# Optimization experiments

Measured on AMD Instinct MI355X. Metric: run time of the kernel, lower is better.

The kernel has to match this reference:

```python
import jax, jax.numpy as jnp
import numpy as np

LAMBDA_SOFTMAX = 10.0  # opt.lambda_softmax
LEAKY_SLOPE = 0.1


def l2norm(x, axis):
    # matches torch F.normalize(p=2, eps=1e-12)
    n = jnp.linalg.norm(x, axis=axis, keepdims=True)
    return x / jnp.clip(n, 1e-12)


def setup_inputs() -> dict:
    key = jax.random.key(0)
    k1, k2, k3, k4, k5 = jax.random.split(key, 5)
    I, Q, T, S, D = 64, 49, 64, 64, 256  # n_img, n_region, n_txt, max_words, feature_size
    return {
        "local_img_query": jax.random.normal(k1, (I, Q, D), jnp.float32),
        "local_img_value": jax.random.normal(k2, (I, Q, D), jnp.float32),
        "local_text_key": jax.random.normal(k3, (T, S, D), jnp.float32),
        "local_text_value": jax.random.normal(k4, (T, S, D), jnp.float32),
        "text_length": jax.random.randint(k5, (T,), 8, S + 1, jnp.int32),
    }


def reference(local_img_query, local_img_value, local_text_key, local_text_value, text_length):
    # Vectorized form of the per-sentence Python loop in compute_i2t_sim.
    # Variable sentence lengths are handled with a mask over the padded word axis,
    # which reproduces the ragged torch math exactly (see comments).
    T, S, D = local_text_key.shape
    I, Q, _ = local_img_query.shape

    qn = l2norm(local_img_query, -1)   # [I,Q,D]
    kn = l2norm(local_text_key, -1)    # [T,S,D]

    # bmm(txt_key_norm, queryT): (B,S,D)x(B,D,Q) -> here [T,I,S,Q]
    attn = jnp.einsum('tsd,iqd->tisq', kn, qn)
    attn = jnp.where(attn > 0, attn, LEAKY_SLOPE * attn)      # LeakyReLU(0.1)
    # l2norm(attn, 2) normalizes over queryL per (t,i,s) row -> independent of padding
    attn = l2norm(attn, -1)
    attn = jnp.swapaxes(attn, 2, 3)                            # [T,I,Q,S]

    mask = jnp.arange(S)[None, :] < text_length[:, None]       # [T,S]
    logits = jnp.where(mask[:, None, None, :], attn * LAMBDA_SOFTMAX, -jnp.inf)
    attn = jax.nn.softmax(logits, axis=-1)                     # padded words -> exactly 0

    # focal_equal with sourceL = actual n_word of each sentence
    n_word = text_length.astype(attn.dtype)[:, None, None, None]
    funcF = attn * n_word - jnp.sum(attn, axis=-1, keepdims=True)
    fattn = (funcF > 0).astype(attn.dtype)                     # padded attn=0 -> funcF<0 -> 0
    tmp = fattn * attn
    attn = tmp / jnp.sum(tmp, axis=-1, keepdims=True)

    # bmm(valueT, attnT) -> weighted text context per (txt, img): [T,I,Q,D]
    wei = jnp.einsum('tsd,tiqs->tiqd', local_text_value, attn)
    wei = l2norm(wei, -1)

    # cosine similarity with image values along d, then mean over regions
    v = local_img_value[None]                                  # [1,I,Q,D]
    w12 = jnp.sum(v * wei, -1)
    denom = jnp.linalg.norm(v, axis=-1) * jnp.linalg.norm(wei, axis=-1)
    sim = w12 / jnp.clip(denom, 1e-8)                          # [T,I,Q]
    i2t = sim.mean(axis=-1)                                    # [T,I]
    return i2t.T                                               # [n_img, n_txt]
```

## Files before the change

kernel.cpp:

```cpp
#include <hip/hip_runtime.h>
#include <math.h>

#define I_N 64
#define Q_N 49
#define T_N 64
#define S_N 64
#define D_N 256

typedef __attribute__((ext_vector_type(8))) short short8;
typedef __attribute__((ext_vector_type(4))) float f32x4;
typedef unsigned short ushort_t;

__device__ __forceinline__ float waveReduceSum64(float v) {
    v += __shfl_xor(v, 1);
    v += __shfl_xor(v, 2);
    v += __shfl_xor(v, 4);
    v += __shfl_xor(v, 8);
    v += __shfl_xor(v, 16);
    v += __shfl_xor(v, 32);
    return v;
}

__device__ __forceinline__ ushort_t f2bf(float x) {
    unsigned u = __builtin_bit_cast(unsigned, x);
    unsigned r = (u + 0x7fffu + ((u >> 16) & 1u)) >> 16;
    return (ushort_t)r;
}
__device__ __forceinline__ float bf2f(ushort_t h) {
    unsigned u = ((unsigned)h) << 16;
    return __builtin_bit_cast(float, u);
}
__device__ __forceinline__ void split_bf16(float x, ushort_t& h, ushort_t& l) {
    h = f2bf(x);
    l = f2bf(x - bf2f(h));
}

__global__ void prep_all(const float* __restrict__ q_in, const float* __restrict__ v_in,
                         const float* __restrict__ k_in, const float* __restrict__ tv,
                         ushort_t* __restrict__ qfh, ushort_t* __restrict__ qfl,
                         ushort_t* __restrict__ kfh, ushort_t* __restrict__ kfl,
                         ushort_t* __restrict__ vfh, ushort_t* __restrict__ vfl,
                         float* __restrict__ vP, float* __restrict__ vnorm) {
    __shared__ float tile[64][65];
    __shared__ float ws[8];
    int b = blockIdx.x;
    int tid = threadIdx.x;

    if (b < 8192) {
        int isimg = (b < 4096) ? 1 : 0;
        int row = isimg ? b : (b - 4096);
        int hi = row >> 6, lo = row & 63;
        float x = 0.0f, vv = 0.0f;
        if (isimg) {
            if (lo < Q_N) {
                size_t base = ((size_t)hi * Q_N + lo) * D_N + tid;
                x = q_in[base];
                vv = v_in[base];
            }
        } else {
            x = k_in[(size_t)row * D_N + tid];
        }
        float s1 = waveReduceSum64(x * x);
        float s2 = waveReduceSum64(vv * vv);
        int wv = tid >> 6, ln = tid & 63;
        if (ln == 0) { ws[wv] = s1; ws[4 + wv] = s2; }
        __syncthreads();
        float n1 = sqrtf(ws[0] + ws[1] + ws[2] + ws[3]);
        float xn = x / fmaxf(n1, 1e-12f);
        ushort_t h, l;
        split_bf16(xn, h, l);
        size_t off = ((size_t)hi << 14) + (size_t)((((lo >> 4) * 8 + (tid >> 5))) << 9)
                   + (size_t)(((((tid >> 3) & 3) * 16 + (lo & 15))) << 3) + (tid & 7);
        if (isimg) {
            qfh[off] = h;
            qfl[off] = l;
            if (tid == 0) vnorm[row] = sqrtf(ws[4] + ws[5] + ws[6] + ws[7]);
        } else {
            kfh[off] = h;
            kfl[off] = l;
        }
    } else if (b < 8448) {
        int bb = b - 8192;
        int t = bb >> 2;
        int d0 = (bb & 3) * 64;
        const float* src = tv + ((size_t)t << 14) + d0;
        ushort_t* dh = vfh + ((size_t)t << 14);
        ushort_t* dl = vfl + ((size_t)t << 14);
#pragma unroll
        for (int r = 0; r < 16; ++r) {
            int idx = r * 256 + tid;
            int s = idx >> 6, d = idx & 63;
            tile[s][d] = src[s * D_N + d];
        }
        __syncthreads();
#pragma unroll
        for (int r = 0; r < 16; ++r) {
            int idx = r * 256 + tid;
            int d = idx >> 6, s = idx & 63;
            int dg = d0 + d;
            float x = tile[s][d];
            ushort_t h, l;
            split_bf16(x, h, l);
            int dgrp = dg >> 4, lrd = dg & 15;
            int k0g = s >> 5, lk3 = (s >> 3) & 3, e = s & 7;
            size_t off = (size_t)(dgrp << 10) + (k0g << 9) + ((lk3 * 16 + lrd) << 3) + e;
            dh[off] = h;
            dl[off] = l;
        }
    } else {
        int i = b - 8448;
        const float* src = v_in + (size_t)i * Q_N * D_N;
        int wv = tid >> 6, lane = tid & 63;
        int lr = lane & 15, lk = lane >> 4;
        float* d0 = vP + ((size_t)i << 14) + (size_t)tid * 64;
#pragma unroll
        for (int nq = 0; nq < 4; ++nq) {
            int q = nq * 16 + lr;
#pragma unroll
            for (int md = 0; md < 4; ++md)
#pragma unroll
                for (int r = 0; r < 4; ++r) {
                    int d = wv * 64 + md * 16 + lk * 4 + r;
                    d0[nq * 16 + md * 4 + r] = (q < Q_N) ? src[q * D_N + d] : 0.0f;
                }
        }
    }
}

__launch_bounds__(256, 3)
__global__ void i2t_mfma(const ushort_t* __restrict__ kfh, const ushort_t* __restrict__ kfl,
                         const ushort_t* __restrict__ qfh, const ushort_t* __restrict__ qfl,
                         const ushort_t* __restrict__ vfh, const ushort_t* __restrict__ vfl,
                         const float* __restrict__ vP,
                         const float* __restrict__ vnorm,
                         const int* __restrict__ tlen,
                         float* __restrict__ out)
{
    __shared__ __align__(16) unsigned char RK[33280];

    const int bid = blockIdx.x;
    const int xcd = bid & 7;
    const int j = bid >> 3;
    const int t = (xcd << 3) | (j & 7);
    const int i = j >> 3;

    const int tid = threadIdx.x;
    const int lane = tid & 63;
    const int w = tid >> 6;
    const int lr = lane & 15;
    const int lk = lane >> 4;

    const int wsr = (w >> 1) * 32;
    const int wq  = (w & 1) * 32;
    f32x4 acc[2][2];
#pragma unroll
    for (int a = 0; a < 2; ++a)
#pragma unroll
        for (int b2 = 0; b2 < 2; ++b2) acc[a][b2] = (f32x4){0.f, 0.f, 0.f, 0.f};
    {
        const ushort_t* kH = kfh + ((size_t)t << 14) + (size_t)(w >> 1) * 8192;
        const ushort_t* kL = kfl + ((size_t)t << 14) + (size_t)(w >> 1) * 8192;
        const ushort_t* qH = qfh + ((size_t)i << 14) + (size_t)(w & 1) * 8192;
        const ushort_t* qL = qfl + ((size_t)i << 14) + (size_t)(w & 1) * 8192;
#pragma unroll
        for (int k8 = 0; k8 < 8; ++k8) {
            int fo = k8 * 512 + lane * 8;
            short8 aH0 = *(const short8*)(kH + fo);
            short8 aL0 = *(const short8*)(kL + fo);
            short8 aH1 = *(const short8*)(kH + 4096 + fo);
            short8 aL1 = *(const short8*)(kL + 4096 + fo);
            short8 bH0 = *(const short8*)(qH + fo);
            short8 bL0 = *(const short8*)(qL + fo);
            short8 bH1 = *(const short8*)(qH + 4096 + fo);
            short8 bL1 = *(const short8*)(qL + 4096 + fo);
            acc[0][0] = __builtin_amdgcn_mfma_f32_16x16x32_bf16(aH0, bH0, acc[0][0], 0, 0, 0);
            acc[0][1] = __builtin_amdgcn_mfma_f32_16x16x32_bf16(aH0, bH1, acc[0][1], 0, 0, 0);
            acc[1][0] = __builtin_amdgcn_mfma_f32_16x16x32_bf16(aH1, bH0, acc[1][0], 0, 0, 0);
            acc[1][1] = __builtin_amdgcn_mfma_f32_16x16x32_bf16(aH1, bH1, acc[1][1], 0, 0, 0);
            acc[0][0] = __builtin_amdgcn_mfma_f32_16x16x32_bf16(aH0, bL0, acc[0][0], 0, 0, 0);
            acc[0][1] = __builtin_amdgcn_mfma_f32_16x16x32_bf16(aH0, bL1, acc[0][1], 0, 0, 0);
            acc[1][0] = __builtin_amdgcn_mfma_f32_16x16x32_bf16(aH1, bL0, acc[1][0], 0, 0, 0);
            acc[1][1] = __builtin_amdgcn_mfma_f32_16x16x32_bf16(aH1, bL1, acc[1][1], 0, 0, 0);
            acc[0][0] = __builtin_amdgcn_mfma_f32_16x16x32_bf16(aL0, bH0, acc[0][0], 0, 0, 0);
            acc[0][1] = __builtin_amdgcn_mfma_f32_16x16x32_bf16(aL0, bH1, acc[0][1], 0, 0, 0);
            acc[1][0] = __builtin_amdgcn_mfma_f32_16x16x32_bf16(aL1, bH0, acc[1][0], 0, 0, 0);
            acc[1][1] = __builtin_amdgcn_mfma_f32_16x16x32_bf16(aL1, bH1, acc[1][1], 0, 0, 0);
        }
    }
    {
        float* As = (float*)RK;
#pragma unroll
        for (int si = 0; si < 2; ++si)
#pragma unroll
            for (int qi = 0; qi < 2; ++qi)
#pragma unroll
                for (int r = 0; r < 4; ++r) {
                    int s = wsr + si * 16 + lk * 4 + r;
                    int q = wq + qi * 16 + lr;
                    float v = acc[si][qi][r];
                    v = (v > 0.0f) ? v : 0.1f * v;
                    As[s * 65 + q] = v;
                }
    }
    __syncthreads();

    {
        const float* As = (const float*)RK;
        float* rinv = (float*)(RK + 16640);
        int s = tid >> 2, part = tid & 3;
        float ss = 0.0f;
#pragma unroll
        for (int q0 = 0; q0 < 64; q0 += 4) {
            float v = As[s * 65 + q0 + part];
            ss += v * v;
        }
        ss += __shfl_xor(ss, 1);
        ss += __shfl_xor(ss, 2);
        if (part == 0) rinv[s] = 1.0f / fmaxf(sqrtf(ss), 1e-12f);
    }
    __syncthreads();

    const int len = tlen[t];
    {
        const float* As = (const float*)RK;
        const float* rinv = (const float*)(RK + 16640);
        ushort_t* Ph = (ushort_t*)(RK + 16896);
        ushort_t* Pl = (ushort_t*)(RK + 25088);
        const float thr = 1.0f / (float)len;
        int q = tid >> 2, part = tid & 3;
        float logit[16];
        float m = -INFINITY;
#pragma unroll
        for (int k = 0; k < 16; ++k) {
            int s = part * 16 + k;
            float lg = (s < len) ? 10.0f * As[s * 65 + q] * rinv[s] : -INFINITY;
            logit[k] = lg;
            m = fmaxf(m, lg);
        }
        m = fmaxf(m, __shfl_xor(m, 1));
        m = fmaxf(m, __shfl_xor(m, 2));
        float p[16];
        float sum = 0.0f;
#pragma unroll
        for (int k = 0; k < 16; ++k) {
            int s = part * 16 + k;
            float e = (s < len) ? __expf(logit[k] - m) : 0.0f;
            p[k] = e;
            sum += e;
        }
        sum += __shfl_xor(sum, 1);
        sum += __shfl_xor(sum, 2);
        float inv = 1.0f / sum;
        float sk = 0.0f;
#pragma unroll
        for (int k = 0; k < 16; ++k) {
            p[k] *= inv;
            if (p[k] > thr) sk += p[k];
        }
        sk += __shfl_xor(sk, 1);
        sk += __shfl_xor(sk, 2);
        float iv2 = 1.0f / sk;

        ushort_t hh[16], ll[16];
#pragma unroll
        for (int k = 0; k < 16; ++k) {
            float pv = (p[k] > thr) ? p[k] * iv2 : 0.0f;
            if (q >= Q_N) pv = 0.0f;
            split_bf16(pv, hh[k], ll[k]);
        }
        int c0 = (2 * part) ^ (q & 7);
        int c1 = (2 * part + 1) ^ (q & 7);
        short8 v0, v1;
#pragma unroll
        for (int k = 0; k < 8; ++k) { v0[k] = (short)hh[k]; v1[k] = (short)hh[k + 8]; }
        *(short8*)(Ph + q * 64 + (c0 << 3)) = v0;
        *(short8*)(Ph + q * 64 + (c1 << 3)) = v1;
#pragma unroll
        for (int k = 0; k < 8; ++k) { v0[k] = (short)ll[k]; v1[k] = (short)ll[k + 8]; }
        *(short8*)(Pl + q * 64 + (c0 << 3)) = v0;
        *(short8*)(Pl + q * 64 + (c1 << 3)) = v1;
    }
    __syncthreads();

    f32x4 acc2[4][4];
#pragma unroll
    for (int a = 0; a < 4; ++a)
#pragma unroll
        for (int b2 = 0; b2 < 4; ++b2) acc2[a][b2] = (f32x4){0.f, 0.f, 0.f, 0.f};
    {
        const ushort_t* vH = vfh + ((size_t)t << 14) + (size_t)w * 4096;
        const ushort_t* vL = vfl + ((size_t)t << 14) + (size_t)w * 4096;
        const ushort_t* PH = (const ushort_t*)(RK + 16896);
        const ushort_t* PL = (const ushort_t*)(RK + 25088);
#pragma unroll
        for (int k0g = 0; k0g < 2; ++k0g) {
#pragma unroll
            for (int md = 0; md < 4; ++md) {
                int vo = md * 1024 + k0g * 512 + lane * 8;
                short8 vh = *(const short8*)(vH + vo);
                short8 vl = *(const short8*)(vL + vo);
#pragma unroll
                for (int nq = 0; nq < 4; ++nq) {
                    int qrow = nq * 16 + lr;
                    int o = qrow * 64 + (((k0g * 4 + lk) ^ (qrow & 7)) << 3);
                    short8 ph = *(const short8*)(PH + o);
                    short8 pl = *(const short8*)(PL + o);
                    acc2[md][nq] = __builtin_amdgcn_mfma_f32_16x16x32_bf16(vh, ph, acc2[md][nq], 0, 0, 0);
                    acc2[md][nq] = __builtin_amdgcn_mfma_f32_16x16x32_bf16(vl, ph, acc2[md][nq], 0, 0, 0);
                    acc2[md][nq] = __builtin_amdgcn_mfma_f32_16x16x32_bf16(vh, pl, acc2[md][nq], 0, 0, 0);
                }
            }
        }
    }

    {
        float* wsq = (float*)RK;
        float* wdv = (float*)(RK + 1024);
        const float* vPb = vP + ((((size_t)i * 4 + w) * 64 + lane) << 6);
#pragma unroll
        for (int nq = 0; nq < 4; ++nq) {
            float s2 = 0.0f, dv = 0.0f;
#pragma unroll
            for (int md = 0; md < 4; ++md) {
                f32x4 vv = *(const f32x4*)(vPb + nq * 16 + md * 4);
#pragma unroll
                for (int r = 0; r < 4; ++r) {
                    float wv = acc2[md][nq][r];
                    s2 += wv * wv;
                    dv += wv * vv[r];
                }
            }
            s2 += __shfl_xor(s2, 16);
            s2 += __shfl_xor(s2, 32);
            dv += __shfl_xor(dv, 16);
            dv += __shfl_xor(dv, 32);
            if (lane < 16) {
                wsq[w * 64 + nq * 16 + lane] = s2;
                wdv[w * 64 + nq * 16 + lane] = dv;
            }
        }
    }
    __syncthreads();
    if (tid < 64) {
        const float* wsq = (const float*)RK;
        const float* wdv = (const float*)(RK + 1024);
        int q = tid;
        float s2 = 0.0f, dv = 0.0f;
#pragma unroll
        for (int ww = 0; ww < 4; ++ww) {
            s2 += wsq[ww * 64 + q];
            dv += wdv[ww * 64 + q];
        }
        float sim = 0.0f;
        if (q < Q_N) {
            float wn = sqrtf(s2);
            float w12 = dv / fmaxf(wn, 1e-12f);
            float wnn = wn / fmaxf(wn, 1e-12f);
            float denom = fmaxf(vnorm[i * 64 + q] * wnn, 1e-8f);
            sim = w12 / denom;
        }
        sim = waveReduceSum64(sim);
        if (tid == 0) out[(size_t)i * T_N + t] = sim * (1.0f / (float)Q_N);
    }
}

extern "C" void kernel_launch(void* const* d_in, const int* in_sizes, int n_in,
                              void* d_out, int out_size, void* d_ws, size_t ws_size,
                              hipStream_t stream) {
    const float* img_query = (const float*)d_in[0];
    const float* img_value = (const float*)d_in[1];
    const float* text_key  = (const float*)d_in[2];
    const float* text_val  = (const float*)d_in[3];
    const int*   text_len  = (const int*)d_in[4];
    float* out = (float*)d_out;

    const size_t NPAD = (size_t)64 * 64 * 256;
    ushort_t* qfh = (ushort_t*)d_ws;
    ushort_t* qfl = qfh + NPAD;
    ushort_t* kfh = qfl + NPAD;
    ushort_t* kfl = kfh + NPAD;
    ushort_t* vfh = kfl + NPAD;
    ushort_t* vfl = vfh + NPAD;
    float* vnorm  = (float*)(vfl + NPAD);
    float* vP     = vnorm + I_N * 64;

    prep_all<<<8512, 256, 0, stream>>>(img_query, img_value, text_key, text_val,
                                       qfh, qfl, kfh, kfl, vfh, vfl, vP, vnorm);

    i2t_mfma<<<T_N * I_N, 256, 0, stream>>>(kfh, kfl, qfh, qfl, vfh, vfl,
                                            vP, vnorm, text_len, out);
}
```

Before: 116.1 us.

## Collapse per-pair block to a single wave with register-resident softmax

The 256-thread block per (text, image) pair becomes a single 64-lane wave. That wave computes the full 64x64 attention tile in MFMA accumulators. LeakyReLU, the row l2norm, the masked softmax and the focal threshold are all done in registers with cross-lane shuffles, so the fp32 staging of attention in LDS and all __syncthreads go away. The second GEMM is looped over four d-chunks inside the wave, and the cosine partials are accumulated in registers. The cost is more serial MFMA work and higher register pressure per wave, with fewer waves available to hide latency.

Result: slower. 126.8 us (+9.2%).

```diff
diff --git a/kernel.cpp b/kernel.cpp
--- a/kernel.cpp
+++ b/kernel.cpp
@@ -8,6 +8,7 @@
 #define D_N 256
 
 typedef __attribute__((ext_vector_type(8))) short short8;
+typedef __attribute__((ext_vector_type(4))) short s16x4;
 typedef __attribute__((ext_vector_type(4))) float f32x4;
 typedef unsigned short ushort_t;
 
@@ -127,8 +128,10 @@
     }
 }
 
-__launch_bounds__(256, 3)
-__global__ void i2t_mfma(const ushort_t* __restrict__ kfh, const ushort_t* __restrict__ kfl,
+#define MFMA16(A, B, C) __builtin_amdgcn_mfma_f32_16x16x32_bf16(A, B, C, 0, 0, 0)
+
+__launch_bounds__(64, 3)
+__global__ void i2t_wave(const ushort_t* __restrict__ kfh, const ushort_t* __restrict__ kfl,
                          const ushort_t* __restrict__ qfh, const ushort_t* __restrict__ qfl,
                          const ushort_t* __restrict__ vfh, const ushort_t* __restrict__ vfl,
                          const float* __restrict__ vP,
@@ -136,7 +139,8 @@
                          const int* __restrict__ tlen,
                          float* __restrict__ out)
 {
-    __shared__ __align__(16) unsigned char RK[33280];
+    __shared__ __align__(16) ushort_t Ph[4096];
+    __shared__ __align__(16) ushort_t Pl[4096];
 
     const int bid = blockIdx.x;
     const int xcd = bid & 7;
@@ -144,213 +148,208 @@
     const int t = (xcd << 3) | (j & 7);
     const int i = j >> 3;
 
-    const int tid = threadIdx.x;
-    const int lane = tid & 63;
-    const int w = tid >> 6;
-    const int lr = lane & 15;
-    const int lk = lane >> 4;
-
-    const int wsr = (w >> 1) * 32;
-    const int wq  = (w & 1) * 32;
-    f32x4 acc[2][2];
-#pragma unroll
-    for (int a = 0; a < 2; ++a)
-#pragma unroll
-        for (int b2 = 0; b2 < 2; ++b2) acc[a][b2] = (f32x4){0.f, 0.f, 0.f, 0.f};
+    const int l = threadIdx.x;
+    const int c16 = l & 15;
+    const int g = l >> 4;
+
+    f32x4 acc[4][4];
+#pragma unroll
+    for (int a = 0; a < 4; ++a)
+#pragma unroll
+        for (int b2 = 0; b2 < 4; ++b2) acc[a][b2] = (f32x4){0.f, 0.f, 0.f, 0.f};
     {
-        const ushort_t* kH = kfh + ((size_t)t << 14) + (size_t)(w >> 1) * 8192;
-        const ushort_t* kL = kfl + ((size_t)t << 14) + (size_t)(w >> 1) * 8192;
-        const ushort_t* qH = qfh + ((size_t)i << 14) + (size_t)(w & 1) * 8192;
-        const ushort_t* qL = qfl + ((size_t)i << 14) + (size_t)(w & 1) * 8192;
+        const ushort_t* kH = kfh + ((size_t)t << 14) + l * 8;
+        const ushort_t* kL = kfl + ((size_t)t << 14) + l * 8;
+        const ushort_t* qH = qfh + ((size_t)i << 14) + l * 8;
+        const ushort_t* qL = qfl + ((size_t)i << 14) + l * 8;
 #pragma unroll
         for (int k8 = 0; k8 < 8; ++k8) {
-            int fo = k8 * 512 + lane * 8;
-            short8 aH0 = *(const short8*)(kH + fo);
-            short8 aL0 = *(const short8*)(kL + fo);
-            short8 aH1 = *(const short8*)(kH + 4096 + fo);
-            short8 aL1 = *(const short8*)(kL + 4096 + fo);
-            short8 bH0 = *(const short8*)(qH + fo);
-            short8 bL0 = *(const short8*)(qL + fo);
-            short8 bH1 = *(const short8*)(qH + 4096 + fo);
-            short8 bL1 = *(const short8*)(qL + 4096 + fo);
-            acc[0][0] = __builtin_amdgcn_mfma_f32_16x16x32_bf16(aH0, bH0, acc[0][0], 0, 0, 0);
-            acc[0][1] = __builtin_amdgcn_mfma_f32_16x16x32_bf16(aH0, bH1, acc[0][1], 0, 0, 0);
-            acc[1][0] = __builtin_amdgcn_mfma_f32_16x16x32_bf16(aH1, bH0, acc[1][0], 0, 0, 0);
-            acc[1][1] = __builtin_amdgcn_mfma_f32_16x16x32_bf16(aH1, bH1, acc[1][1], 0, 0, 0);
-            acc[0][0] = __builtin_amdgcn_mfma_f32_16x16x32_bf16(aH0, bL0, acc[0][0], 0, 0, 0);
-            acc[0][1] = __builtin_amdgcn_mfma_f32_16x16x32_bf16(aH0, bL1, acc[0][1], 0, 0, 0);
-            acc[1][0] = __builtin_amdgcn_mfma_f32_16x16x32_bf16(aH1, bL0, acc[1][0], 0, 0, 0);
-            acc[1][1] = __builtin_amdgcn_mfma_f32_16x16x32_bf16(aH1, bL1, acc[1][1], 0, 0, 0);
-            acc[0][0] = __builtin_amdgcn_mfma_f32_16x16x32_bf16(aL0, bH0, acc[0][0], 0, 0, 0);
-            acc[0][1] = __builtin_amdgcn_mfma_f32_16x16x32_bf16(aL0, bH1, acc[0][1], 0, 0, 0);
-            acc[1][0] = __builtin_amdgcn_mfma_f32_16x16x32_bf16(aL1, bH0, acc[1][0], 0, 0, 0);
-            acc[1][1] = __builtin_amdgcn_mfma_f32_16x16x32_bf16(aL1, bH1, acc[1][1], 0, 0, 0);
-        }
-    }
+            short8 bH[4], bL[4];
+#pragma unroll
+            for (int qi = 0; qi < 4; ++qi) {
+                int o = (qi * 8 + k8) * 512;
+                bH[qi] = *(const short8*)(qH + o);
+                bL[qi] = *(const short8*)(qL + o);
+            }
+#pragma unroll
+            for (int si = 0; si < 4; ++si) {
+                int o = (si * 8 + k8) * 512;
+                short8 aH = *(const short8*)(kH + o);
+                short8 aL = *(const short8*)(kL + o);
+#pragma unroll
+                for (int qi = 0; qi < 4; ++qi) {
+                    acc[si][qi] = MFMA16(aH, bH[qi], acc[si][qi]);
+                    acc[si][qi] = MFMA16(aH, bL[qi], acc[si][qi]);
+                    acc[si][qi] = MFMA16(aL, bH[qi], acc[si][qi]);
+                }
+            }
+        }
+    }
+
+    const int len = tlen[t];
+    const float thr = 1.0f / (float)len;
+#pragma unroll
+    for (int si = 0; si < 4; ++si)
+#pragma unroll
+        for (int qi = 0; qi < 4; ++qi)
+#pragma unroll
+            for (int r = 0; r < 4; ++r) {
+                float v = acc[si][qi][r];
+                acc[si][qi][r] = (v > 0.0f) ? v : 0.1f * v;
+            }
     {
-        float* As = (float*)RK;
-#pragma unroll
-        for (int si = 0; si < 2; ++si)
-#pragma unroll
-            for (int qi = 0; qi < 2; ++qi)
-#pragma unroll
-                for (int r = 0; r < 4; ++r) {
-                    int s = wsr + si * 16 + lk * 4 + r;
-                    int q = wq + qi * 16 + lr;
+        float rv[4][4];
+#pragma unroll
+        for (int si = 0; si < 4; ++si)
+#pragma unroll
+            for (int r = 0; r < 4; ++r) {
+                float ss = 0.0f;
+#pragma unroll
+                for (int qi = 0; qi < 4; ++qi) {
                     float v = acc[si][qi][r];
-                    v = (v > 0.0f) ? v : 0.1f * v;
-                    As[s * 65 + q] = v;
-                }
-    }
-    __syncthreads();
-
-    {
-        const float* As = (const float*)RK;
-        float* rinv = (float*)(RK + 16640);
-        int s = tid >> 2, part = tid & 3;
-        float ss = 0.0f;
-#pragma unroll
-        for (int q0 = 0; q0 < 64; q0 += 4) {
-            float v = As[s * 65 + q0 + part];
-            ss += v * v;
-        }
-        ss += __shfl_xor(ss, 1);
-        ss += __shfl_xor(ss, 2);
-        if (part == 0) rinv[s] = 1.0f / fmaxf(sqrtf(ss), 1e-12f);
-    }
-    __syncthreads();
-
-    const int len = tlen[t];
-    {
-        const float* As = (const float*)RK;
-        const float* rinv = (const float*)(RK + 16640);
-        ushort_t* Ph = (ushort_t*)(RK + 16896);
-        ushort_t* Pl = (ushort_t*)(RK + 25088);
-        const float thr = 1.0f / (float)len;
-        int q = tid >> 2, part = tid & 3;
-        float logit[16];
+                    ss += v * v;
+                }
+                ss += __shfl_xor(ss, 1);
+                ss += __shfl_xor(ss, 2);
+                ss += __shfl_xor(ss, 4);
+                ss += __shfl_xor(ss, 8);
+                rv[si][r] = 10.0f / fmaxf(sqrtf(ss), 1e-12f);
+            }
+#pragma unroll
+        for (int si = 0; si < 4; ++si)
+#pragma unroll
+            for (int qi = 0; qi < 4; ++qi)
+#pragma unroll
+                for (int r = 0; r < 4; ++r) acc[si][qi][r] *= rv[si][r];
+    }
+#pragma unroll
+    for (int qi = 0; qi < 4; ++qi) {
         float m = -INFINITY;
 #pragma unroll
-        for (int k = 0; k < 16; ++k) {
-            int s = part * 16 + k;
-            float lg = (s < len) ? 10.0f * As[s * 65 + q] * rinv[s] : -INFINITY;
-            logit[k] = lg;
-            m = fmaxf(m, lg);
-        }
-        m = fmaxf(m, __shfl_xor(m, 1));
-        m = fmaxf(m, __shfl_xor(m, 2));
-        float p[16];
+        for (int si = 0; si < 4; ++si)
+#pragma unroll
+            for (int r = 0; r < 4; ++r) {
+                int s = si * 16 + g * 4 + r;
+                float lg = (s < len) ? acc[si][qi][r] : -INFINITY;
+                m = fmaxf(m, lg);
+            }
+        m = fmaxf(m, __shfl_xor(m, 16));
+        m = fmaxf(m, __shfl_xor(m, 32));
         float sum = 0.0f;
 #pragma unroll
-        for (int k = 0; k < 16; ++k) {
-            int s = part * 16 + k;
-            float e = (s < len) ? __expf(logit[k] - m) : 0.0f;
-            p[k] = e;
-            sum += e;
-        }
-        sum += __shfl_xor(sum, 1);
-        sum += __shfl_xor(sum, 2);
+        for (int si = 0; si < 4; ++si)
+#pragma unroll
+            for (int r = 0; r < 4; ++r) {
+                int s = si * 16 + g * 4 + r;
+                float e = (s < len) ? __expf(acc[si][qi][r] - m) : 0.0f;
+                acc[si][qi][r] = e;
+                sum += e;
+            }
+        sum += __shfl_xor(sum, 16);
+        sum += __shfl_xor(sum, 32);
         float inv = 1.0f / sum;
         float sk = 0.0f;
 #pragma unroll
-        for (int k = 0; k < 16; ++k) {
-            p[k] *= inv;
-            if (p[k] > thr) sk += p[k];
-        }
-        sk += __shfl_xor(sk, 1);
-        sk += __shfl_xor(sk, 2);
+        for (int si = 0; si < 4; ++si)
+#pragma unroll
+            for (int r = 0; r < 4; ++r) {
+                float p = acc[si][qi][r] * inv;
+                acc[si][qi][r] = p;
+                if (p > thr) sk += p;
+            }
+        sk += __shfl_xor(sk, 16);
+        sk += __shfl_xor(sk, 32);
         float iv2 = 1.0f / sk;
-
-        ushort_t hh[16], ll[16];
-#pragma unroll
-        for (int k = 0; k < 16; ++k) {
-            float pv = (p[k] > thr) ? p[k] * iv2 : 0.0f;
-            if (q >= Q_N) pv = 0.0f;
-            split_bf16(pv, hh[k], ll[k]);
-        }
-        int c0 = (2 * part) ^ (q & 7);
-        int c1 = (2 * part + 1) ^ (q & 7);
-        short8 v0, v1;
-#pragma unroll
-        for (int k = 0; k < 8; ++k) { v0[k] = (short)hh[k]; v1[k] = (short)hh[k + 8]; }
-        *(short8*)(Ph + q * 64 + (c0 << 3)) = v0;
-        *(short8*)(Ph + q * 64 + (c1 << 3)) = v1;
-#pragma unroll
-        for (int k = 0; k < 8; ++k) { v0[k] = (short)ll[k]; v1[k] = (short)ll[k + 8]; }
-        *(short8*)(Pl + q * 64 + (c0 << 3)) = v0;
-        *(short8*)(Pl + q * 64 + (c1 << 3)) = v1;
-    }
-    __syncthreads();
-
-    f32x4 acc2[4][4];
-#pragma unroll
-    for (int a = 0; a < 4; ++a)
-#pragma unroll
-        for (int b2 = 0; b2 < 4; ++b2) acc2[a][b2] = (f32x4){0.f, 0.f, 0.f, 0.f};
+        bool qok = (qi * 16 + c16) < Q_N;
+#pragma unroll
+        for (int si = 0; si < 4; ++si)
+#pragma unroll
+            for (int r = 0; r < 4; ++r) {
+                float p = acc[si][qi][r];
+                p = (p > thr) ? p * iv2 : 0.0f;
+                if (!qok) p = 0.0f;
+                acc[si][qi][r] = p;
+            }
+    }
+
+#pragma unroll
+    for (int si = 0; si < 4; ++si)
+#pragma unroll
+        for (int qi = 0; qi < 4; ++qi) {
+            int q = qi * 16 + c16;
+            int s0 = si * 16 + g * 4;
+            int cidx = s0 >> 3;
+            int off = q * 64 + ((cidx ^ (q & 7)) << 3) + (g & 1) * 4;
+            s16x4 vh, vl;
+#pragma unroll
+            for (int r = 0; r < 4; ++r) {
+                ushort_t hh, ll;
+                split_bf16(acc[si][qi][r], hh, ll);
+                vh[r] = (short)hh;
+                vl[r] = (short)ll;
+            }
+            *(s16x4*)(Ph + off) = vh;
+            *(s16x4*)(Pl + off) = vl;
+        }
+    __asm__ volatile("s_waitcnt lgkmcnt(0)" ::: "memory");
+    __builtin_amdgcn_sched_barrier(0);
+
+    float s2a[4] = {0.f, 0.f, 0.f, 0.f}, dva[4] = {0.f, 0.f, 0.f, 0.f};
     {
-        const ushort_t* vH = vfh + ((size_t)t << 14) + (size_t)w * 4096;
-        const ushort_t* vL = vfl + ((size_t)t << 14) + (size_t)w * 4096;
-        const ushort_t* PH = (const ushort_t*)(RK + 16896);
-        const ushort_t* PL = (const ushort_t*)(RK + 25088);
-#pragma unroll
-        for (int k0g = 0; k0g < 2; ++k0g) {
-#pragma unroll
-            for (int md = 0; md < 4; ++md) {
-                int vo = md * 1024 + k0g * 512 + lane * 8;
-                short8 vh = *(const short8*)(vH + vo);
-                short8 vl = *(const short8*)(vL + vo);
-#pragma unroll
-                for (int nq = 0; nq < 4; ++nq) {
-                    int qrow = nq * 16 + lr;
-                    int o = qrow * 64 + (((k0g * 4 + lk) ^ (qrow & 7)) << 3);
-                    short8 ph = *(const short8*)(PH + o);
-                    short8 pl = *(const short8*)(PL + o);
-                    acc2[md][nq] = __builtin_amdgcn_mfma_f32_16x16x32_bf16(vh, ph, acc2[md][nq], 0, 0, 0);
-                    acc2[md][nq] = __builtin_amdgcn_mfma_f32_16x16x32_bf16(vl, ph, acc2[md][nq], 0, 0, 0);
-                    acc2[md][nq] = __builtin_amdgcn_mfma_f32_16x16x32_bf16(vh, pl, acc2[md][nq], 0, 0, 0);
-                }
-            }
-        }
-    }
-
-    {
-        float* wsq = (float*)RK;
-        float* wdv = (float*)(RK + 1024);
-        const float* vPb = vP + ((((size_t)i * 4 + w) * 64 + lane) << 6);
-#pragma unroll
-        for (int nq = 0; nq < 4; ++nq) {
-            float s2 = 0.0f, dv = 0.0f;
-#pragma unroll
-            for (int md = 0; md < 4; ++md) {
-                f32x4 vv = *(const f32x4*)(vPb + nq * 16 + md * 4);
-#pragma unroll
-                for (int r = 0; r < 4; ++r) {
-                    float wv = acc2[md][nq][r];
-                    s2 += wv * wv;
-                    dv += wv * vv[r];
-                }
-            }
-            s2 += __shfl_xor(s2, 16);
-            s2 += __shfl_xor(s2, 32);
-            dv += __shfl_xor(dv, 16);
-            dv += __shfl_xor(dv, 32);
-            if (lane < 16) {
-                wsq[w * 64 + nq * 16 + lane] = s2;
-                wdv[w * 64 + nq * 16 + lane] = dv;
-            }
-        }
-    }
-    __syncthreads();
-    if (tid < 64) {
-        const float* wsq = (const float*)RK;
-        const float* wdv = (const float*)(RK + 1024);
-        int q = tid;
-        float s2 = 0.0f, dv = 0.0f;
-#pragma unroll
-        for (int ww = 0; ww < 4; ++ww) {
-            s2 += wsq[ww * 64 + q];
-            dv += wdv[ww * 64 + q];
-        }
+        const ushort_t* vH = vfh + ((size_t)t << 14) + l * 8;
+        const ushort_t* vL = vfl + ((size_t)t << 14) + l * 8;
+#pragma unroll
+        for (int dc = 0; dc < 4; ++dc) {
+            f32x4 acc2[4][4];
+#pragma unroll
+            for (int a = 0; a < 4; ++a)
+#pragma unroll
+                for (int b2 = 0; b2 < 4; ++b2) acc2[a][b2] = (f32x4){0.f, 0.f, 0.f, 0.f};
+#pragma unroll
+            for (int k0g = 0; k0g < 2; ++k0g) {
+#pragma unroll
+                for (int md = 0; md < 4; ++md) {
+                    int vo = (dc * 4 + md) * 1024 + k0g * 512;
+                    short8 vh = *(const short8*)(vH + vo);
+                    short8 vl = *(const short8*)(vL + vo);
+#pragma unroll
+                    for (int nq = 0; nq < 4; ++nq) {
+                        int q = nq * 16 + c16;
+                        int o = q * 64 + (((k0g * 4 + g) ^ (q & 7)) << 3);
+                        short8 ph = *(const short8*)(Ph + o);
+                        short8 pl = *(const short8*)(Pl + o);
+                        acc2[md][nq] = MFMA16(vh, ph, acc2[md][nq]);
+                        acc2[md][nq] = MFMA16(vl, ph, acc2[md][nq]);
+                        acc2[md][nq] = MFMA16(vh, pl, acc2[md][nq]);
+                    }
+                }
+            }
+            const float* vPc = vP + ((((size_t)i * 4 + dc) * 64 + l) << 6);
+#pragma unroll
+            for (int nq = 0; nq < 4; ++nq) {
+#pragma unroll
+                for (int md = 0; md < 4; ++md) {
+                    f32x4 vv = *(const f32x4*)(vPc + nq * 16 + md * 4);
+#pragma unroll
+                    for (int r = 0; r < 4; ++r) {
+                        float w = acc2[md][nq][r];
+                        s2a[nq] += w * w;
+                        dva[nq] += w * vv[r];
+                    }
+                }
+            }
+        }
+    }
+
+    float res = 0.0f;
+#pragma unroll
+    for (int nq = 0; nq < 4; ++nq) {
+        float s2 = s2a[nq], dv = dva[nq];
+        s2 += __shfl_xor(s2, 16);
+        s2 += __shfl_xor(s2, 32);
+        dv += __shfl_xor(dv, 16);
+        dv += __shfl_xor(dv, 32);
+        int q = nq * 16 + c16;
         float sim = 0.0f;
         if (q < Q_N) {
             float wn = sqrtf(s2);
@@ -359,9 +358,10 @@
             float denom = fmaxf(vnorm[i * 64 + q] * wnn, 1e-8f);
             sim = w12 / denom;
         }
-        sim = waveReduceSum64(sim);
-        if (tid == 0) out[(size_t)i * T_N + t] = sim * (1.0f / (float)Q_N);
-    }
+        res += sim;
+    }
+    res = waveReduceSum64(res);
+    if (l == 0) out[(size_t)i * T_N + t] = res * (0.25f / (float)Q_N);
 }
 
 extern "C" void kernel_launch(void* const* d_in, const int* in_sizes, int n_in,
@@ -387,6 +387,6 @@
     prep_all<<<8512, 256, 0, stream>>>(img_query, img_value, text_key, text_val,
                                        qfh, qfl, kfh, kfl, vfh, vfl, vP, vnorm);
 
-    i2t_mfma<<<T_N * I_N, 256, 0, stream>>>(kfh, kfl, qfh, qfl, vfh, vfl,
-                                            vP, vnorm, text_len, out);
-}
+    i2t_wave<<<T_N * I_N, 64, 0, stream>>>(kfh, kfl, qfh, qfl, vfh, vfl,
+                                           vP, vnorm, text_len, out);
+}
```

## Process two images per block to reuse text key fragments

Applied to the files above, without the earlier changes.

Each block now handles one text and two images, loading the text key fragments once and running the first GEMM for both images in the same loop. The softmax, second GEMM and cosine epilogue are factored into a helper that runs sequentially for each image, with an extra barrier between them. The grid is halved. The aim is to cut redundant key loads and block launch overhead, at the cost of more accumulator registers, less parallelism (2048 blocks), and a longer serial chain inside each block.

Measured after the change: 112.4 us. 3.2% less time.

```diff
diff --git a/kernel.cpp b/kernel.cpp
--- a/kernel.cpp
+++ b/kernel.cpp
@@ -127,6 +127,195 @@
     }
 }
 
+__device__ __forceinline__ void process_image(
+    f32x4 a00, f32x4 a01, f32x4 a10, f32x4 a11,
+    unsigned char* RK,
+    const ushort_t* __restrict__ vfh, const ushort_t* __restrict__ vfl,
+    const float* __restrict__ vP, const float* __restrict__ vnorm,
+    float* __restrict__ out, int t, int i, int len, int tid)
+{
+    const int lane = tid & 63;
+    const int w = tid >> 6;
+    const int lr = lane & 15;
+    const int lk = lane >> 4;
+    const int wsr = (w >> 1) * 32;
+    const int wq  = (w & 1) * 32;
+
+    {
+        float* As = (float*)RK;
+#pragma unroll
+        for (int r = 0; r < 4; ++r) {
+            int s = wsr + lk * 4 + r;
+            int q = wq + lr;
+            float v;
+            v = a00[r]; As[s * 65 + q]            = (v > 0.0f) ? v : 0.1f * v;
+            v = a01[r]; As[s * 65 + q + 16]       = (v > 0.0f) ? v : 0.1f * v;
+            v = a10[r]; As[(s + 16) * 65 + q]     = (v > 0.0f) ? v : 0.1f * v;
+            v = a11[r]; As[(s + 16) * 65 + q + 16] = (v > 0.0f) ? v : 0.1f * v;
+        }
+    }
+    __syncthreads();
+
+    {
+        const float* As = (const float*)RK;
+        float* rinv = (float*)(RK + 16640);
+        int s = tid >> 2, part = tid & 3;
+        float ss = 0.0f;
+#pragma unroll
+        for (int q0 = 0; q0 < 64; q0 += 4) {
+            float v = As[s * 65 + q0 + part];
+            ss += v * v;
+        }
+        ss += __shfl_xor(ss, 1);
+        ss += __shfl_xor(ss, 2);
+        if (part == 0) rinv[s] = 1.0f / fmaxf(sqrtf(ss), 1e-12f);
+    }
+    __syncthreads();
+
+    {
+        const float* As = (const float*)RK;
+        const float* rinv = (const float*)(RK + 16640);
+        ushort_t* Ph = (ushort_t*)(RK + 16896);
+        ushort_t* Pl = (ushort_t*)(RK + 25088);
+        const float thr = 1.0f / (float)len;
+        int q = tid >> 2, part = tid & 3;
+        float logit[16];
+        float m = -INFINITY;
+#pragma unroll
+        for (int k = 0; k < 16; ++k) {
+            int s = part * 16 + k;
+            float lg = (s < len) ? 10.0f * As[s * 65 + q] * rinv[s] : -INFINITY;
+            logit[k] = lg;
+            m = fmaxf(m, lg);
+        }
+        m = fmaxf(m, __shfl_xor(m, 1));
+        m = fmaxf(m, __shfl_xor(m, 2));
+        float p[16];
+        float sum = 0.0f;
+#pragma unroll
+        for (int k = 0; k < 16; ++k) {
+            int s = part * 16 + k;
+            float e = (s < len) ? __expf(logit[k] - m) : 0.0f;
+            p[k] = e;
+            sum += e;
+        }
+        sum += __shfl_xor(sum, 1);
+        sum += __shfl_xor(sum, 2);
+        float inv = 1.0f / sum;
+        float sk = 0.0f;
+#pragma unroll
+        for (int k = 0; k < 16; ++k) {
+            p[k] *= inv;
+            if (p[k] > thr) sk += p[k];
+        }
+        sk += __shfl_xor(sk, 1);
+        sk += __shfl_xor(sk, 2);
+        float iv2 = 1.0f / sk;
+
+        ushort_t hh[16], ll[16];
+#pragma unroll
+        for (int k = 0; k < 16; ++k) {
+            float pv = (p[k] > thr) ? p[k] * iv2 : 0.0f;
+            if (q >= Q_N) pv = 0.0f;
+            split_bf16(pv, hh[k], ll[k]);
+        }
+        int c0 = (2 * part) ^ (q & 7);
+        int c1 = (2 * part + 1) ^ (q & 7);
+        short8 v0, v1;
+#pragma unroll
+        for (int k = 0; k < 8; ++k) { v0[k] = (short)hh[k]; v1[k] = (short)hh[k + 8]; }
+        *(short8*)(Ph + q * 64 + (c0 << 3)) = v0;
+        *(short8*)(Ph + q * 64 + (c1 << 3)) = v1;
+#pragma unroll
+        for (int k = 0; k < 8; ++k) { v0[k] = (short)ll[k]; v1[k] = (short)ll[k + 8]; }
+        *(short8*)(Pl + q * 64 + (c0 << 3)) = v0;
+        *(short8*)(Pl + q * 64 + (c1 << 3)) = v1;
+    }
+    __syncthreads();
+
+    f32x4 acc2[4][4];
+#pragma unroll
+    for (int a = 0; a < 4; ++a)
+#pragma unroll
+        for (int b2 = 0; b2 < 4; ++b2) acc2[a][b2] = (f32x4){0.f, 0.f, 0.f, 0.f};
+    {
+        const ushort_t* vH = vfh + ((size_t)t << 14) + (size_t)w * 4096;
+        const ushort_t* vL = vfl + ((size_t)t << 14) + (size_t)w * 4096;
+        const ushort_t* PH = (const ushort_t*)(RK + 16896);
+        const ushort_t* PL = (const ushort_t*)(RK + 25088);
+#pragma unroll
+        for (int k0g = 0; k0g < 2; ++k0g) {
+#pragma unroll
+            for (int md = 0; md < 4; ++md) {
+                int vo = md * 1024 + k0g * 512 + lane * 8;
+                short8 vh = *(const short8*)(vH + vo);
+                short8 vl = *(const short8*)(vL + vo);
+#pragma unroll
+                for (int nq = 0; nq < 4; ++nq) {
+                    int qrow = nq * 16 + lr;
+                    int o = qrow * 64 + (((k0g * 4 + lk) ^ (qrow & 7)) << 3);
+                    short8 ph = *(const short8*)(PH + o);
+                    short8 pl = *(const short8*)(PL + o);
+                    acc2[md][nq] = __builtin_amdgcn_mfma_f32_16x16x32_bf16(vh, ph, acc2[md][nq], 0, 0, 0);
+                    acc2[md][nq] = __builtin_amdgcn_mfma_f32_16x16x32_bf16(vl, ph, acc2[md][nq], 0, 0, 0);
+                    acc2[md][nq] = __builtin_amdgcn_mfma_f32_16x16x32_bf16(vh, pl, acc2[md][nq], 0, 0, 0);
+                }
+            }
+        }
+    }
+
+    {
+        float* wsq = (float*)RK;
+        float* wdv = (float*)(RK + 1024);
+        const float* vPb = vP + ((((size_t)i * 4 + w) * 64 + lane) << 6);
+#pragma unroll
+        for (int nq = 0; nq < 4; ++nq) {
+            float s2 = 0.0f, dv = 0.0f;
+#pragma unroll
+            for (int md = 0; md < 4; ++md) {
+                f32x4 vv = *(const f32x4*)(vPb + nq * 16 + md * 4);
+#pragma unroll
+                for (int r = 0; r < 4; ++r) {
+                    float wv = acc2[md][nq][r];
+                    s2 += wv * wv;
+                    dv += wv * vv[r];
+                }
+            }
+            s2 += __shfl_xor(s2, 16);
+            s2 += __shfl_xor(s2, 32);
+            dv += __shfl_xor(dv, 16);
+            dv += __shfl_xor(dv, 32);
+            if (lane < 16) {
+                wsq[w * 64 + nq * 16 + lane] = s2;
+                wdv[w * 64 + nq * 16 + lane] = dv;
+            }
+        }
+    }
+    __syncthreads();
+    if (tid < 64) {
+        const float* wsq = (const float*)RK;
+        const float* wdv = (const float*)(RK + 1024);
+        int q = tid;
+        float s2 = 0.0f, dv = 0.0f;
+#pragma unroll
+        for (int ww = 0; ww < 4; ++ww) {
+            s2 += wsq[ww * 64 + q];
+            dv += wdv[ww * 64 + q];
+        }
+        float sim = 0.0f;
+        if (q < Q_N) {
+            float wn = sqrtf(s2);
+            float w12 = dv / fmaxf(wn, 1e-12f);
+            float wnn = wn / fmaxf(wn, 1e-12f);
+            float denom = fmaxf(vnorm[i * 64 + q] * wnn, 1e-8f);
+            sim = w12 / denom;
+        }
+        sim = waveReduceSum64(sim);
+        if (tid == 0) out[(size_t)i * T_N + t] = sim * (1.0f / (float)Q_N);
+    }
+    __syncthreads();
+}
+
 __launch_bounds__(256, 3)
 __global__ void i2t_mfma(const ushort_t* __restrict__ kfh, const ushort_t* __restrict__ kfl,
                          const ushort_t* __restrict__ qfh, const ushort_t* __restrict__ qfl,
@@ -142,26 +331,28 @@
     const int xcd = bid & 7;
     const int j = bid >> 3;
     const int t = (xcd << 3) | (j & 7);
-    const int i = j >> 3;
+    const int ip = j >> 3;
+    const int i0 = 2 * ip, i1 = 2 * ip + 1;
 
     const int tid = threadIdx.x;
     const int lane = tid & 63;
     const int w = tid >> 6;
-    const int lr = lane & 15;
-    const int lk = lane >> 4;
-
-    const int wsr = (w >> 1) * 32;
-    const int wq  = (w & 1) * 32;
-    f32x4 acc[2][2];
+
+    f32x4 accA[2][2], accB[2][2];
 #pragma unroll
     for (int a = 0; a < 2; ++a)
 #pragma unroll
-        for (int b2 = 0; b2 < 2; ++b2) acc[a][b2] = (f32x4){0.f, 0.f, 0.f, 0.f};
-    {
-        const ushort_t* kH = kfh + ((size_t)t << 14) + (size_t)(w >> 1) * 8192;
-        const ushort_t* kL = kfl + ((size_t)t << 14) + (size_t)(w >> 1) * 8192;
-        const ushort_t* qH = qfh + ((size_t)i << 14) + (size_t)(w & 1) * 8192;
-        const ushort_t* qL = qfl + ((size_t)i << 14) + (size_t)(w & 1) * 8192;
+        for (int b2 = 0; b2 < 2; ++b2) {
+            accA[a][b2] = (f32x4){0.f, 0.f, 0.f, 0.f};
+            accB[a][b2] = (f32x4){0.f, 0.f, 0.f, 0.f};
+        }
+    {
+        const ushort_t* kH  = kfh + ((size_t)t << 14) + (size_t)(w >> 1) * 8192;
+        const ushort_t* kL  = kfl + ((size_t)t << 14) + (size_t)(w >> 1) * 8192;
+        const ushort_t* q0H = qfh + ((size_t)i0 << 14) + (size_t)(w & 1) * 8192;
+        const ushort_t* q0L = qfl + ((size_t)i0 << 14) + (size_t)(w & 1) * 8192;
+        const ushort_t* q1H = qfh + ((size_t)i1 << 14) + (size_t)(w & 1) * 8192;
+        const ushort_t* q1L = qfl + ((size_t)i1 << 14) + (size_t)(w & 1) * 8192;
 #pragma unroll
         for (int k8 = 0; k8 < 8; ++k8) {
             int fo = k8 * 512 + lane * 8;
@@ -169,199 +360,50 @@
             short8 aL0 = *(const short8*)(kL + fo);
             short8 aH1 = *(const short8*)(kH + 4096 + fo);
             short8 aL1 = *(const short8*)(kL + 4096 + fo);
-            short8 bH0 = *(const short8*)(qH + fo);
-            short8 bL0 = *(const short8*)(qL + fo);
-            short8 bH1 = *(const short8*)(qH + 4096 + fo);
-            short8 bL1 = *(const short8*)(qL + 4096 + fo);
-            acc[0][0] = __builtin_amdgcn_mfma_f32_16x16x32_bf16(aH0, bH0, acc[0][0], 0, 0, 0);
-            acc[0][1] = __builtin_amdgcn_mfma_f32_16x16x32_bf16(aH0, bH1, acc[0][1], 0, 0, 0);
-            acc[1][0] = __builtin_amdgcn_mfma_f32_16x16x32_bf16(aH1, bH0, acc[1][0], 0, 0, 0);
-            acc[1][1] = __builtin_amdgcn_mfma_f32_16x16x32_bf16(aH1, bH1, acc[1][1], 0, 0, 0);
-            acc[0][0] = __builtin_amdgcn_mfma_f32_16x16x32_bf16(aH0, bL0, acc[0][0], 0, 0, 0);
-            acc[0][1] = __builtin_amdgcn_mfma_f32_16x16x32_bf16(aH0, bL1, acc[0][1], 0, 0, 0);
-            acc[1][0] = __builtin_amdgcn_mfma_f32_16x16x32_bf16(aH1, bL0, acc[1][0], 0, 0, 0);
-            acc[1][1] = __builtin_amdgcn_mfma_f32_16x16x32_bf16(aH1, bL1, acc[1][1], 0, 0, 0);
-            acc[0][0] = __builtin_amdgcn_mfma_f32_16x16x32_bf16(aL0, bH0, acc[0][0], 0, 0, 0);
-            acc[0][1] = __builtin_amdgcn_mfma_f32_16x16x32_bf16(aL0, bH1, acc[0][1], 0, 0, 0);
-            acc[1][0] = __builtin_amdgcn_mfma_f32_16x16x32_bf16(aL1, bH0, acc[1][0], 0, 0, 0);
-            acc[1][1] = __builtin_amdgcn_mfma_f32_16x16x32_bf16(aL1, bH1, acc[1][1], 0, 0, 0);
-        }
-    }
-    {
-        float* As = (float*)RK;
-#pragma unroll
-        for (int si = 0; si < 2; ++si)
-#pragma unroll
-            for (int qi = 0; qi < 2; ++qi)
-#pragma unroll
-                for (int r = 0; r < 4; ++r) {
-                    int s = wsr + si * 16 + lk * 4 + r;
-                    int q = wq + qi * 16 + lr;
-                    float v = acc[si][qi][r];
-                    v = (v > 0.0f) ? v : 0.1f * v;
-                    As[s * 65 + q] = v;
-                }
-    }
-    __syncthreads();
-
-    {
-        const float* As = (const float*)RK;
-        float* rinv = (float*)(RK + 16640);
-        int s = tid >> 2, part = tid & 3;
-        float ss = 0.0f;
-#pragma unroll
-        for (int q0 = 0; q0 < 64; q0 += 4) {
-            float v = As[s * 65 + q0 + part];
-            ss += v * v;
-        }
-        ss += __shfl_xor(ss, 1);
-        ss += __shfl_xor(ss, 2);
-        if (part == 0) rinv[s] = 1.0f / fmaxf(sqrtf(ss), 1e-12f);
-    }
-    __syncthreads();
+            {
+                short8 bH0 = *(const short8*)(q0H + fo);
+                short8 bL0 = *(const short8*)(q0L + fo);
+                short8 bH1 = *(const short8*)(q0H + 4096 + fo);
+                short8 bL1 = *(const short8*)(q0L + 4096 + fo);
+                accA[0][0] = __builtin_amdgcn_mfma_f32_16x16x32_bf16(aH0, bH0, accA[0][0], 0, 0, 0);
+                accA[0][1] = __builtin_amdgcn_mfma_f32_16x16x32_bf16(aH0, bH1, accA[0][1], 0, 0, 0);
+                accA[1][0] = __builtin_amdgcn_mfma_f32_16x16x32_bf16(aH1, bH0, accA[1][0], 0, 0, 0);
+                accA[1][1] = __builtin_amdgcn_mfma_f32_16x16x32_bf16(aH1, bH1, accA[1][1], 0, 0, 0);
+                accA[0][0] = __builtin_amdgcn_mfma_f32_16x16x32_bf16(aH0, bL0, accA[0][0], 0, 0, 0);
+                accA[0][1] = __builtin_amdgcn_mfma_f32_16x16x32_bf16(aH0, bL1, accA[0][1], 0, 0, 0);
+                accA[1][0] = __builtin_amdgcn_mfma_f32_16x16x32_bf16(aH1, bL0, accA[1][0], 0, 0, 0);
+                accA[1][1] = __builtin_amdgcn_mfma_f32_16x16x32_bf16(aH1, bL1, accA[1][1], 0, 0, 0);
+                accA[0][0] = __builtin_amdgcn_mfma_f32_16x16x32_bf16(aL0, bH0, accA[0][0], 0, 0, 0);
+                accA[0][1] = __builtin_amdgcn_mfma_f32_16x16x32_bf16(aL0, bH1, accA[0][1], 0, 0, 0);
+                accA[1][0] = __builtin_amdgcn_mfma_f32_16x16x32_bf16(aL1, bH0, accA[1][0], 0, 0, 0);
+                accA[1][1] = __builtin_amdgcn_mfma_f32_16x16x32_bf16(aL1, bH1, accA[1][1], 0, 0, 0);
+            }
+            {
+                short8 bH0 = *(const short8*)(q1H + fo);
+                short8 bL0 = *(const short8*)(q1L + fo);
+                short8 bH1 = *(const short8*)(q1H + 4096 + fo);
+                short8 bL1 = *(const short8*)(q1L + 4096 + fo);
+                accB[0][0] = __builtin_amdgcn_mfma_f32_16x16x32_bf16(aH0, bH0, accB[0][0], 0, 0, 0);
+                accB[0][1] = __builtin_amdgcn_mfma_f32_16x16x32_bf16(aH0, bH1, accB[0][1], 0, 0, 0);
+                accB[1][0] = __builtin_amdgcn_mfma_f32_16x16x32_bf16(aH1, bH0, accB[1][0], 0, 0, 0);
+                accB[1][1] = __builtin_amdgcn_mfma_f32_16x16x32_bf16(aH1, bH1, accB[1][1], 0, 0, 0);
+                accB[0][0] = __builtin_amdgcn_mfma_f32_16x16x32_bf16(aH0, bL0, accB[0][0], 0, 0, 0);
+                accB[0][1] = __builtin_amdgcn_mfma_f32_16x16x32_bf16(aH0, bL1, accB[0][1], 0, 0, 0);
+                accB[1][0] = __builtin_amdgcn_mfma_f32_16x16x32_bf16(aH1, bL0, accB[1][0], 0, 0, 0);
+                accB[1][1] = __builtin_amdgcn_mfma_f32_16x16x32_bf16(aH1, bL1, accB[1][1], 0, 0, 0);
+                accB[0][0] = __builtin_amdgcn_mfma_f32_16x16x32_bf16(aL0, bH0, accB[0][0], 0, 0, 0);
+                accB[0][1] = __builtin_amdgcn_mfma_f32_16x16x32_bf16(aL0, bH1, accB[0][1], 0, 0, 0);
+                accB[1][0] = __builtin_amdgcn_mfma_f32_16x16x32_bf16(aL1, bH0, accB[1][0], 0, 0, 0);
+                accB[1][1] = __builtin_amdgcn_mfma_f32_16x16x32_bf16(aL1, bH1, accB[1][1], 0, 0, 0);
+            }
+        }
+    }
 
     const int len = tlen[t];
-    {
-        const float* As = (const float*)RK;
-        const float* rinv = (const float*)(RK + 16640);
-        ushort_t* Ph = (ushort_t*)(RK + 16896);
-        ushort_t* Pl = (ushort_t*)(RK + 25088);
-        const float thr = 1.0f / (float)len;
-        int q = tid >> 2, part = tid & 3;
-        float logit[16];
-        float m = -INFINITY;
-#pragma unroll
-        for (int k = 0; k < 16; ++k) {
-            int s = part * 16 + k;
-            float lg = (s < len) ? 10.0f * As[s * 65 + q] * rinv[s] : -INFINITY;
-            logit[k] = lg;
-            m = fmaxf(m, lg);
-        }
-        m = fmaxf(m, __shfl_xor(m, 1));
-        m = fmaxf(m, __shfl_xor(m, 2));
-        float p[16];
-        float sum = 0.0f;
-#pragma unroll
-        for (int k = 0; k < 16; ++k) {
-            int s = part * 16 + k;
-            float e = (s < len) ? __expf(logit[k] - m) : 0.0f;
-            p[k] = e;
-            sum += e;
-        }
-        sum += __shfl_xor(sum, 1);
-        sum += __shfl_xor(sum, 2);
-        float inv = 1.0f / sum;
-        float sk = 0.0f;
-#pragma unroll
-        for (int k = 0; k < 16; ++k) {
-            p[k] *= inv;
-            if (p[k] > thr) sk += p[k];
-        }
-        sk += __shfl_xor(sk, 1);
-        sk += __shfl_xor(sk, 2);
-        float iv2 = 1.0f / sk;
-
-        ushort_t hh[16], ll[16];
-#pragma unroll
-        for (int k = 0; k < 16; ++k) {
-            float pv = (p[k] > thr) ? p[k] * iv2 : 0.0f;
-            if (q >= Q_N) pv = 0.0f;
-            split_bf16(pv, hh[k], ll[k]);
-        }
-        int c0 = (2 * part) ^ (q & 7);
-        int c1 = (2 * part + 1) ^ (q & 7);
-        short8 v0, v1;
-#pragma unroll
-        for (int k = 0; k < 8; ++k) { v0[k] = (short)hh[k]; v1[k] = (short)hh[k + 8]; }
-        *(short8*)(Ph + q * 64 + (c0 << 3)) = v0;
-        *(short8*)(Ph + q * 64 + (c1 << 3)) = v1;
-#pragma unroll
-        for (int k = 0; k < 8; ++k) { v0[k] = (short)ll[k]; v1[k] = (short)ll[k + 8]; }
-        *(short8*)(Pl + q * 64 + (c0 << 3)) = v0;
-        *(short8*)(Pl + q * 64 + (c1 << 3)) = v1;
-    }
-    __syncthreads();
-
-    f32x4 acc2[4][4];
-#pragma unroll
-    for (int a = 0; a < 4; ++a)
-#pragma unroll
-        for (int b2 = 0; b2 < 4; ++b2) acc2[a][b2] = (f32x4){0.f, 0.f, 0.f, 0.f};
-    {
-        const ushort_t* vH = vfh + ((size_t)t << 14) + (size_t)w * 4096;
-        const ushort_t* vL = vfl + ((size_t)t << 14) + (size_t)w * 4096;
-        const ushort_t* PH = (const ushort_t*)(RK + 16896);
-        const ushort_t* PL = (const ushort_t*)(RK + 25088);
-#pragma unroll
-        for (int k0g = 0; k0g < 2; ++k0g) {
-#pragma unroll
-            for (int md = 0; md < 4; ++md) {
-                int vo = md * 1024 + k0g * 512 + lane * 8;
-                short8 vh = *(const short8*)(vH + vo);
-                short8 vl = *(const short8*)(vL + vo);
-#pragma unroll
-                for (int nq = 0; nq < 4; ++nq) {
-                    int qrow = nq * 16 + lr;
-                    int o = qrow * 64 + (((k0g * 4 + lk) ^ (qrow & 7)) << 3);
-                    short8 ph = *(const short8*)(PH + o);
-                    short8 pl = *(const short8*)(PL + o);
-                    acc2[md][nq] = __builtin_amdgcn_mfma_f32_16x16x32_bf16(vh, ph, acc2[md][nq], 0, 0, 0);
-                    acc2[md][nq] = __builtin_amdgcn_mfma_f32_16x16x32_bf16(vl, ph, acc2[md][nq], 0, 0, 0);
-                    acc2[md][nq] = __builtin_amdgcn_mfma_f32_16x16x32_bf16(vh, pl, acc2[md][nq], 0, 0, 0);
-                }
-            }
-        }
-    }
-
-    {
-        float* wsq = (float*)RK;
-        float* wdv = (float*)(RK + 1024);
-        const float* vPb = vP + ((((size_t)i * 4 + w) * 64 + lane) << 6);
-#pragma unroll
-        for (int nq = 0; nq < 4; ++nq) {
-            float s2 = 0.0f, dv = 0.0f;
-#pragma unroll
-            for (int md = 0; md < 4; ++md) {
-                f32x4 vv = *(const f32x4*)(vPb + nq * 16 + md * 4);
-#pragma unroll
-                for (int r = 0; r < 4; ++r) {
-                    float wv = acc2[md][nq][r];
-                    s2 += wv * wv;
-                    dv += wv * vv[r];
-                }
-            }
-            s2 += __shfl_xor(s2, 16);
-            s2 += __shfl_xor(s2, 32);
-            dv += __shfl_xor(dv, 16);
-            dv += __shfl_xor(dv, 32);
-            if (lane < 16) {
-                wsq[w * 64 + nq * 16 + lane] = s2;
-                wdv[w * 64 + nq * 16 + lane] = dv;
-            }
-        }
-    }
-    __syncthreads();
-    if (tid < 64) {
-        const float* wsq = (const float*)RK;
-        const float* wdv = (const float*)(RK + 1024);
-        int q = tid;
-        float s2 = 0.0f, dv = 0.0f;
-#pragma unroll
-        for (int ww = 0; ww < 4; ++ww) {
-            s2 += wsq[ww * 64 + q];
-            dv += wdv[ww * 64 + q];
-        }
-        float sim = 0.0f;
-        if (q < Q_N) {
-            float wn = sqrtf(s2);
-            float w12 = dv / fmaxf(wn, 1e-12f);
-            float wnn = wn / fmaxf(wn, 1e-12f);
-            float denom = fmaxf(vnorm[i * 64 + q] * wnn, 1e-8f);
-            sim = w12 / denom;
-        }
-        sim = waveReduceSum64(sim);
-        if (tid == 0) out[(size_t)i * T_N + t] = sim * (1.0f / (float)Q_N);
-    }
+    process_image(accA[0][0], accA[0][1], accA[1][0], accA[1][1],
+                  RK, vfh, vfl, vP, vnorm, out, t, i0, len, tid);
+    process_image(accB[0][0], accB[0][1], accB[1][0], accB[1][1],
+                  RK, vfh, vfl, vP, vnorm, out, t, i1, len, tid);
 }
 
 extern "C" void kernel_launch(void* const* d_in, const int* in_sizes, int n_in,
@@ -387,6 +429,6 @@
     prep_all<<<8512, 256, 0, stream>>>(img_query, img_value, text_key, text_val,
                                        qfh, qfl, kfh, kfl, vfh, vfl, vP, vnorm);
 
-    i2t_mfma<<<T_N * I_N, 256, 0, stream>>>(kfh, kfl, qfh, qfl, vfh, vfl,
-                                            vP, vnorm, text_len, out);
-}
+    i2t_mfma<<<T_N * I_N / 2, 256, 0, stream>>>(kfh, kfl, qfh, qfl, vfh, vfl,
+                                                vP, vnorm, text_len, out);
+}
```
